# Kernel optimization log

Hardware: AMD Instinct MI355X
Metric: run time of the kernel (lower is better)

The kernel has to match this reference:

```python
import jax, jax.numpy as jnp
import numpy as np

_KX = jnp.array([[1., 0., -1.], [2., 0., -2.], [1., 0., -1.]], dtype=jnp.float32).reshape(1, 1, 3, 3)
_KY = jnp.transpose(_KX, (0, 1, 3, 2))  # ky = kx.transpose(2,3)


def _sobel(x, k):
    # x: [B,1,H,W], k: [1,1,3,3]; SAME padding=1, stride 1
    return jax.lax.conv_general_dilated(
        x, k, window_strides=(1, 1), padding=((1, 1), (1, 1)),
        dimension_numbers=('NCHW', 'OIHW', 'NCHW'))


def setup_inputs() -> dict:
    key = jax.random.key(0)
    k1, k2 = jax.random.split(key)
    sr = jax.random.normal(k1, (32, 1, 1024, 1024), dtype=jnp.float32)
    hr = jax.random.normal(k2, (32, 1, 1024, 1024), dtype=jnp.float32)
    return {"sr": sr, "hr": hr}


def reference(sr, hr):
    gx_sr = _sobel(sr, _KX)
    gy_sr = _sobel(sr, _KY)
    gx_hr = _sobel(hr, _KX)
    gy_hr = _sobel(hr, _KY)
    return jnp.mean(jnp.abs(gx_sr - gx_hr) + jnp.abs(gy_sr - gy_hr))
```

## Files before the change

### kernel.cpp

```cpp
#include <hip/hip_runtime.h>


#define IMG_H 1024
#define IMG_W 1024
#define IMG_B 32
#define CH 8
#define NROW (CH + 2)
#define NCHUNK (IMG_H / CH)

__device__ __forceinline__ void row_st(const float4& a, const float4& b,
                                       float ha, float hb, float m, float hm,
                                       int lane, float4& s, float4& t) {
    float4 d;
    d.x = (a.x - b.x) * m;
    d.y = (a.y - b.y) * m;
    d.z = (a.z - b.z) * m;
    d.w = (a.w - b.w) * m;
    const float dh = (ha - hb) * (m * hm);
    float dl = __shfl_up(d.w, 1, 64);
    float dr = __shfl_down(d.x, 1, 64);
    if (lane == 0)  dl = dh;
    if (lane == 63) dr = dh;
    s.x = dl  + 2.f * d.x + d.y;
    s.y = d.x + 2.f * d.y + d.z;
    s.z = d.y + 2.f * d.z + d.w;
    s.w = d.z + 2.f * d.w + dr;
    t.x = dl  - d.y;
    t.y = d.x - d.z;
    t.z = d.y - d.w;
    t.w = d.z - dr;
}

__global__ __launch_bounds__(256, 2) void edge_loss_kernel(
        const float* __restrict__ sr, const float* __restrict__ hr,
        float* __restrict__ out, float invN) {
    const int chunk = blockIdx.x;
    const int b     = blockIdx.y;
    const int tid   = threadIdx.x;
    const int lane  = tid & 63;
    const int x0    = tid * 4;
    const size_t img = (size_t)b * IMG_H * IMG_W;
    const int y0 = chunk * CH;

    const bool isL = (lane == 0);
    const bool isR = (lane == 63);
    const int  hx  = isL ? x0 - 1 : x0 + 4;
    const float hm = (isL ? (x0 > 0) : (x0 + 4 < IMG_W)) ? 1.f : 0.f;
    const int  hxc = min(max(hx, 0), IMG_W - 1);

    float4 A[NROW], B[NROW];
    float  hA[NROW], hB[NROW];
    #pragma unroll
    for (int i = 0; i < NROW; ++i) { hA[i] = 0.f; hB[i] = 0.f; }

    #pragma unroll
    for (int i = 0; i < NROW; ++i) {
        const int yc = min(max(y0 - 1 + i, 0), IMG_H - 1);
        const size_t row = img + (size_t)yc * IMG_W;
        A[i] = *reinterpret_cast<const float4*>(sr + row + x0);
        B[i] = *reinterpret_cast<const float4*>(hr + row + x0);
    }
    if (isL || isR) {
        #pragma unroll
        for (int i = 0; i < NROW; ++i) {
            const int yc = min(max(y0 - 1 + i, 0), IMG_H - 1);
            const size_t row = img + (size_t)yc * IMG_W;
            hA[i] = sr[row + hxc];
            hB[i] = hr[row + hxc];
        }
    }

    __builtin_amdgcn_sched_barrier(0);

    const float mtop = (y0 > 0) ? 1.f : 0.f;
    const float mbot = (y0 + CH < IMG_H) ? 1.f : 0.f;

    float4 s0, t0, s1, t1, s2, t2;
    row_st(A[0], B[0], hA[0], hB[0], mtop, hm, lane, s0, t0);
    row_st(A[1], B[1], hA[1], hB[1], 1.f,  hm, lane, s1, t1);

    float acc = 0.f;
    #pragma unroll
    for (int i = 2; i < NROW; ++i) {
        const float m = (i == NROW - 1) ? mbot : 1.f;
        row_st(A[i], B[i], hA[i], hB[i], m, hm, lane, s2, t2);

        float gx, gy;
        gx = t0.x + 2.f * t1.x + t2.x;  gy = s0.x - s2.x;  acc += fabsf(gx) + fabsf(gy);
        gx = t0.y + 2.f * t1.y + t2.y;  gy = s0.y - s2.y;  acc += fabsf(gx) + fabsf(gy);
        gx = t0.z + 2.f * t1.z + t2.z;  gy = s0.z - s2.z;  acc += fabsf(gx) + fabsf(gy);
        gx = t0.w + 2.f * t1.w + t2.w;  gy = s0.w - s2.w;  acc += fabsf(gx) + fabsf(gy);

        s0 = s1; t0 = t1; s1 = s2; t1 = t2;
    }

    #pragma unroll
    for (int off = 32; off > 0; off >>= 1)
        acc += __shfl_down(acc, off, 64);

    __shared__ float wsum[4];
    const int wave = tid >> 6;
    if (lane == 0) wsum[wave] = acc;
    __syncthreads();
    if (tid == 0) {
        const float bsum = wsum[0] + wsum[1] + wsum[2] + wsum[3];
        atomicAdd(out, bsum * invN);
    }
}

extern "C" void kernel_launch(void* const* d_in, const int* in_sizes, int n_in,
                              void* d_out, int out_size, void* d_ws, size_t ws_size,
                              hipStream_t stream) {
    const float* sr = (const float*)d_in[0];
    const float* hr = (const float*)d_in[1];
    float* out = (float*)d_out;

    hipMemsetAsync(out, 0, sizeof(float), stream);

    dim3 grid(NCHUNK, IMG_B);
    const float invN = 1.0f / (float)((size_t)IMG_B * IMG_H * IMG_W);
    edge_loss_kernel<<<grid, 256, 0, stream>>>(sr, hr, out, invN);
}
```

Before: 276.8 us.

## Stage row tiles into LDS via direct global-to-LDS loads

Replaces the per-thread register loads and cross-lane shuffles with global_load_lds DMA copies of the 10 input rows of both images into shared memory. Each thread then reads its float4 and its left/right halo neighbours from LDS, which removes the separate halo loads and shuffle logic. This costs 80 KB of LDS per block, which limits occupancy, and adds a block barrier before compute.

```diff
diff --git a/kernel.cpp b/kernel.cpp
--- a/kernel.cpp
+++ b/kernel.cpp
@@ -8,19 +8,22 @@
 #define NROW (CH + 2)
 #define NCHUNK (IMG_H / CH)
 
-__device__ __forceinline__ void row_st(const float4& a, const float4& b,
-                                       float ha, float hb, float m, float hm,
-                                       int lane, float4& s, float4& t) {
+#define GLOBAL_PTR(p) ((const __attribute__((address_space(1))) void*)(p))
+#define LDS_PTR(p)    ((__attribute__((address_space(3))) void*)(p))
+
+__device__ __forceinline__ void row_st_lds(const float* __restrict__ a,
+                                           const float* __restrict__ b,
+                                           int x0, float m,
+                                           float4& s, float4& t) {
+    const float4 av = *reinterpret_cast<const float4*>(a + x0);
+    const float4 bv = *reinterpret_cast<const float4*>(b + x0);
     float4 d;
-    d.x = (a.x - b.x) * m;
-    d.y = (a.y - b.y) * m;
-    d.z = (a.z - b.z) * m;
-    d.w = (a.w - b.w) * m;
-    const float dh = (ha - hb) * (m * hm);
-    float dl = __shfl_up(d.w, 1, 64);
-    float dr = __shfl_down(d.x, 1, 64);
-    if (lane == 0)  dl = dh;
-    if (lane == 63) dr = dh;
+    d.x = (av.x - bv.x) * m;
+    d.y = (av.y - bv.y) * m;
+    d.z = (av.z - bv.z) * m;
+    d.w = (av.w - bv.w) * m;
+    const float dl = (x0 > 0)           ? (a[x0 - 1] - b[x0 - 1]) * m : 0.f;
+    const float dr = (x0 + 4 < IMG_W)   ? (a[x0 + 4] - b[x0 + 4]) * m : 0.f;
     s.x = dl  + 2.f * d.x + d.y;
     s.y = d.x + 2.f * d.y + d.z;
     s.z = d.y + 2.f * d.z + d.w;
@@ -31,59 +34,43 @@
     t.w = d.z - dr;
 }
 
-__global__ __launch_bounds__(256, 2) void edge_loss_kernel(
+__global__ __launch_bounds__(256) void edge_loss_kernel(
         const float* __restrict__ sr, const float* __restrict__ hr,
         float* __restrict__ out, float invN) {
+    __shared__ __align__(16) float lA[NROW][IMG_W];
+    __shared__ __align__(16) float lB[NROW][IMG_W];
+
     const int chunk = blockIdx.x;
     const int b     = blockIdx.y;
     const int tid   = threadIdx.x;
     const int lane  = tid & 63;
+    const int wave  = tid >> 6;
     const int x0    = tid * 4;
+    const int wseg  = wave * 256;
     const size_t img = (size_t)b * IMG_H * IMG_W;
     const int y0 = chunk * CH;
 
-    const bool isL = (lane == 0);
-    const bool isR = (lane == 63);
-    const int  hx  = isL ? x0 - 1 : x0 + 4;
-    const float hm = (isL ? (x0 > 0) : (x0 + 4 < IMG_W)) ? 1.f : 0.f;
-    const int  hxc = min(max(hx, 0), IMG_W - 1);
-
-    float4 A[NROW], B[NROW];
-    float  hA[NROW], hB[NROW];
     #pragma unroll
-    for (int i = 0; i < NROW; ++i) { hA[i] = 0.f; hB[i] = 0.f; }
-
-    #pragma unroll
-    for (int i = 0; i < NROW; ++i) {
-        const int yc = min(max(y0 - 1 + i, 0), IMG_H - 1);
-        const size_t row = img + (size_t)yc * IMG_W;
-        A[i] = *reinterpret_cast<const float4*>(sr + row + x0);
-        B[i] = *reinterpret_cast<const float4*>(hr + row + x0);
+    for (int r = 0; r < NROW; ++r) {
+        const int yc = min(max(y0 - 1 + r, 0), IMG_H - 1);
+        const size_t off = img + (size_t)yc * IMG_W + wseg + lane * 4;
+        __builtin_amdgcn_global_load_lds(GLOBAL_PTR(sr + off), LDS_PTR(&lA[r][wseg]), 16, 0, 0);
+        __builtin_amdgcn_global_load_lds(GLOBAL_PTR(hr + off), LDS_PTR(&lB[r][wseg]), 16, 0, 0);
     }
-    if (isL || isR) {
-        #pragma unroll
-        for (int i = 0; i < NROW; ++i) {
-            const int yc = min(max(y0 - 1 + i, 0), IMG_H - 1);
-            const size_t row = img + (size_t)yc * IMG_W;
-            hA[i] = sr[row + hxc];
-            hB[i] = hr[row + hxc];
-        }
-    }
-
-    __builtin_amdgcn_sched_barrier(0);
+    __syncthreads();
 
     const float mtop = (y0 > 0) ? 1.f : 0.f;
     const float mbot = (y0 + CH < IMG_H) ? 1.f : 0.f;
 
     float4 s0, t0, s1, t1, s2, t2;
-    row_st(A[0], B[0], hA[0], hB[0], mtop, hm, lane, s0, t0);
-    row_st(A[1], B[1], hA[1], hB[1], 1.f,  hm, lane, s1, t1);
+    row_st_lds(lA[0], lB[0], x0, mtop, s0, t0);
+    row_st_lds(lA[1], lB[1], x0, 1.f,  s1, t1);
 
     float acc = 0.f;
     #pragma unroll
     for (int i = 2; i < NROW; ++i) {
         const float m = (i == NROW - 1) ? mbot : 1.f;
-        row_st(A[i], B[i], hA[i], hB[i], m, hm, lane, s2, t2);
+        row_st_lds(lA[i], lB[i], x0, m, s2, t2);
 
         float gx, gy;
         gx = t0.x + 2.f * t1.x + t2.x;  gy = s0.x - s2.x;  acc += fabsf(gx) + fabsf(gy);
@@ -98,12 +85,11 @@
     for (int off = 32; off > 0; off >>= 1)
         acc += __shfl_down(acc, off, 64);
 
-    __shared__ float wsum[4];
-    const int wave = tid >> 6;
-    if (lane == 0) wsum[wave] = acc;
+    __syncthreads();
+    if (lane == 0) lA[0][wave] = acc;
     __syncthreads();
     if (tid == 0) {
-        const float bsum = wsum[0] + wsum[1] + wsum[2] + wsum[3];
+        const float bsum = lA[0][0] + lA[0][1] + lA[0][2] + lA[0][3];
         atomicAdd(out, bsum * invN);
     }
 }
```

New measurement: 278.3 us. About the same (+0.5%).
